# Kernel tuning notes

Hardware: AMD Instinct MI355X
Metric: run time of the kernel (lower is better)

## Reference

```python
import jax, jax.numpy as jnp
import numpy as np
import math

NUM_HEADS = 16
HEAD_DIM = 64
NUM_BUCKETS = 256
MAX_DISTANCE = 16384
ROPE_BASE = 10000.0


def _rel_pos_bucket(rel):
    # faithful to RelativePositionEncoding._relative_position_bucket
    ab = jnp.abs(rel)
    max_exact = NUM_BUCKETS // 4  # 64
    half = NUM_BUCKETS // 2       # 128
    is_small = ab < max_exact
    safe = jnp.maximum(ab, 1).astype(jnp.float32)
    large = max_exact + (jnp.log(safe / max_exact) / math.log(MAX_DISTANCE / max_exact) * (half - max_exact)).astype(jnp.int32)
    large = jnp.minimum(large, half - 1)
    bucket = jnp.where(is_small, ab, large)
    bucket = jnp.where(rel < 0, half + bucket, bucket)
    return bucket


def _rope_cos_sin(seq_len):
    # RotaryPositionEncoding with rope dim = 2*head_dim: num_features = head_dim,
    # inv_freq over arange(0, head_dim, 2)/head_dim, interleaved repeat to head_dim
    inv_freq = 1.0 / (ROPE_BASE ** (jnp.arange(0, HEAD_DIM, 2, dtype=jnp.float32) / HEAD_DIM))
    pos = jnp.arange(seq_len, dtype=jnp.float32)
    freqs = pos[:, None] * inv_freq[None, :]          # [S, HEAD_DIM//2]
    cos = jnp.repeat(jnp.cos(freqs), 2, axis=-1)      # [S, HEAD_DIM]
    sin = jnp.repeat(jnp.sin(freqs), 2, axis=-1)
    return cos, sin


def _rotate_half(t):
    h = t.shape[-1] // 2
    return jnp.concatenate([-t[..., h:], t[..., :h]], axis=-1)


def setup_inputs() -> dict:
    key = jax.random.key(0)
    ks = jax.random.split(key, 6)
    B, S, E = 2, 2048, 1024
    x = jax.random.normal(ks[0], (B, S, E), dtype=jnp.float32)
    Wq = jax.random.normal(ks[1], (E, E), dtype=jnp.float32) * 0.02
    Wk = jax.random.normal(ks[2], (E, E), dtype=jnp.float32) * 0.02
    Wv = jax.random.normal(ks[3], (E, E), dtype=jnp.float32) * 0.02
    Wo = jax.random.normal(ks[4], (E, E), dtype=jnp.float32) * 0.02
    rel_emb = jax.random.normal(ks[5], (NUM_BUCKETS, NUM_HEADS, HEAD_DIM), dtype=jnp.float32) * 0.02
    return {"x": x, "Wq": Wq, "Wk": Wk, "Wv": Wv, "Wo": Wo, "rel_emb": rel_emb}


def reference(x, Wq, Wk, Wv, Wo, rel_emb):
    B, S, E = x.shape
    H, D = NUM_HEADS, HEAD_DIM

    def split_heads(t):
        return t.reshape(B, S, H, D).transpose(0, 2, 1, 3)  # [B,H,S,D]

    q = split_heads(x @ Wq)
    k = split_heads(x @ Wk)
    v = split_heads(x @ Wv)

    # inline RoPE on q/k (cos/sin broadcast over batch & heads)
    cos, sin = _rope_cos_sin(S)  # [S, D]
    q = q * cos + _rotate_half(q) * sin
    k = k * cos + _rotate_half(k) * sin

    # relative-position bucket bias: q . rel_emb[bucket(i-j)]
    pos = jnp.arange(S)
    bucket = _rel_pos_bucket(pos[:, None] - pos[None, :])      # [S, S]
    q_rel = jnp.einsum('bhqd,nhd->bhqn', q, rel_emb)           # [B,H,S,NUM_BUCKETS]
    bias = jnp.take_along_axis(q_rel, bucket[None, None, :, :], axis=-1)  # [B,H,S,S]

    scale = 1.0 / math.sqrt(D)
    scores = (jnp.einsum('bhqd,bhkd->bhqk', q, k) + bias) * scale

    causal = pos[:, None] >= pos[None, :]
    scores = jnp.where(causal[None, None], scores, jnp.float32(-1e9))
    attn = jax.nn.softmax(scores, axis=-1)

    out = jnp.einsum('bhqk,bhkd->bhqd', attn, v)
    out = out.transpose(0, 2, 1, 3).reshape(B, S, E)
    return out @ Wo
```

## Files before the change

### kernel.cpp

```cpp
#include <hip/hip_runtime.h>
#include <hip/hip_bf16.h>
#include <math.h>


typedef __attribute__((ext_vector_type(8))) short bf16x8;
typedef __attribute__((ext_vector_type(4))) float f32x4;

static __device__ __forceinline__ unsigned short f2bf(float x) {
    unsigned u = __float_as_uint(x);
    unsigned r = (u + 0x7fffu + ((u >> 16) & 1u)) >> 16;
    return (unsigned short)r;
}
static __device__ __forceinline__ float bf2f(unsigned short h) {
    return __uint_as_float(((unsigned)h) << 16);
}

#define GLOAD16(gp, lp)                                                            \
    __builtin_amdgcn_global_load_lds(                                              \
        (const __attribute__((address_space(1))) unsigned int*)(gp),               \
        (__attribute__((address_space(3))) unsigned int*)(lp), 16, 0, 0)

__global__ void tobf16(const float* __restrict__ in, unsigned short* __restrict__ out)
{
    const size_t t = (size_t)blockIdx.x * 256 + threadIdx.x;
    const float4* p = (const float4*)(in + t*8);
    float4 a = p[0], b = p[1];
    unsigned w0 = f2bf(a.x) | ((unsigned)f2bf(a.y) << 16);
    unsigned w1 = f2bf(a.z) | ((unsigned)f2bf(a.w) << 16);
    unsigned w2 = f2bf(b.x) | ((unsigned)f2bf(b.y) << 16);
    unsigned w3 = f2bf(b.z) | ((unsigned)f2bf(b.w) << 16);
    *(uint4*)(out + t*8) = make_uint4(w0, w1, w2, w3);
}

__global__ void transp4(const float* __restrict__ W0, const float* __restrict__ W1,
                        const float* __restrict__ W2, const float* __restrict__ W3,
                        unsigned short* __restrict__ T0, unsigned short* __restrict__ T1,
                        unsigned short* __restrict__ T2, unsigned short* __restrict__ T3)
{
    const int z = blockIdx.y;
    const float* W = (z == 0) ? W0 : (z == 1) ? W1 : (z == 2) ? W2 : W3;
    unsigned short* Wt = (z == 0) ? T0 : (z == 1) ? T1 : (z == 2) ? T2 : T3;

    __shared__ unsigned short tls[64][65];
    const int tid = threadIdx.x;
    const int bxt = blockIdx.x & 15;
    const int byt = blockIdx.x >> 4;
    const int r   = tid >> 2;
    const int c0  = (tid & 3) * 16;
    const float* src = W + (size_t)(byt*64 + r)*1024 + bxt*64 + c0;
#pragma unroll
    for (int j = 0; j < 4; ++j) {
        float4 vv = ((const float4*)src)[j];
        tls[c0 + j*4 + 0][r] = f2bf(vv.x);
        tls[c0 + j*4 + 1][r] = f2bf(vv.y);
        tls[c0 + j*4 + 2][r] = f2bf(vv.z);
        tls[c0 + j*4 + 3][r] = f2bf(vv.w);
    }
    __syncthreads();
    unsigned short* dst = Wt + (size_t)(bxt*64 + r)*1024 + byt*64 + c0;
    unsigned w[8];
#pragma unroll
    for (int j = 0; j < 8; ++j)
        w[j] = (unsigned)tls[r][c0 + 2*j] | ((unsigned)tls[r][c0 + 2*j + 1] << 16);
    *(uint4*)(dst)     = make_uint4(w[0], w[1], w[2], w[3]);
    *(uint4*)(dst + 8) = make_uint4(w[4], w[5], w[6], w[7]);
}

__global__ void relT_bf(const float* __restrict__ rel, unsigned short* __restrict__ relTb)
{
    const int t  = blockIdx.x * 256 + threadIdx.x;
    const int d0 = (t & 7) * 8;
    const int n  = (t >> 3) & 127;
    const int h  = t >> 10;
    const float* src = rel + ((size_t)(n*16 + h))*64 + d0;
    float4 a = ((const float4*)src)[0], b = ((const float4*)src)[1];
    unsigned w0 = f2bf(a.x) | ((unsigned)f2bf(a.y) << 16);
    unsigned w1 = f2bf(a.z) | ((unsigned)f2bf(a.w) << 16);
    unsigned w2 = f2bf(b.x) | ((unsigned)f2bf(b.y) << 16);
    unsigned w3 = f2bf(b.z) | ((unsigned)f2bf(b.w) << 16);
    *(uint4*)(relTb + (size_t)h*8192 + n*64 + d0) = make_uint4(w0, w1, w2, w3);
}

#define GEMM_STAGE(t, buf)                                                             \
    {                                                                                  \
        const int k0s = (t) * 64;                                                      \
        _Pragma("unroll")                                                              \
        for (int j = 0; j < 4; ++j) {                                                  \
            GLOAD16(agp + (size_t)(j*32 + srow)*1024 + k0s, &Als[buf][0] + j*2048 + tid*8); \
            GLOAD16(bgp + (size_t)(j*32 + srow)*1024 + k0s, &Bls[buf][0] + j*2048 + tid*8); \
        }                                                                              \
    }

#define GEMM_COMPUTE(buf)                                                              \
    {                                                                                  \
        _Pragma("unroll")                                                              \
        for (int ks = 0; ks < 2; ++ks) {                                               \
            bf16x8 af[4], bfr[4];                                                      \
            _Pragma("unroll")                                                          \
            for (int m = 0; m < 4; ++m)                                                \
                af[m] = *(const bf16x8*)&Als[buf][(wr + m*16 + (lane & 15))*64 + ks*32 + (lane >> 4)*8]; \
            _Pragma("unroll")                                                          \
            for (int n = 0; n < 4; ++n)                                                \
                bfr[n] = *(const bf16x8*)&Bls[buf][(wc + n*16 + (lane & 15))*64 + ks*32 + (lane >> 4)*8]; \
            _Pragma("unroll")                                                          \
            for (int m = 0; m < 4; ++m)                                                \
                _Pragma("unroll")                                                      \
                for (int n = 0; n < 4; ++n)                                            \
                    acc[m][n] = __builtin_amdgcn_mfma_f32_16x16x32_bf16(af[m], bfr[n], acc[m][n], 0, 0, 0); \
        }                                                                              \
    }

__global__ __launch_bounds__(256) void gemm_qkv(const unsigned short* __restrict__ A,
    const unsigned short* __restrict__ wtq, const unsigned short* __restrict__ wtk,
    const unsigned short* __restrict__ wtv,
    float* __restrict__ qf, float* __restrict__ kf, unsigned short* __restrict__ vTb)
{
    __shared__ __align__(16) unsigned short Als[2][8192];
    __shared__ __align__(16) unsigned short Bls[2][8192];
    const int z = blockIdx.z;
    const unsigned short* Bt = (z == 0) ? wtq : (z == 1) ? wtk : wtv;

    const int tid  = threadIdx.x;
    const int wave = tid >> 6, lane = tid & 63;
    const int wr = (wave >> 1) * 64, wc = (wave & 1) * 64;
    const int bx = blockIdx.x, by = blockIdx.y;
    const int srow = tid >> 3;
    const unsigned short* agp = A  + (size_t)(by*128)*1024 + (tid & 7)*8;
    const unsigned short* bgp = Bt + (size_t)(bx*128)*1024 + (tid & 7)*8;

    f32x4 acc[4][4];
#pragma unroll
    for (int m = 0; m < 4; ++m)
#pragma unroll
        for (int n = 0; n < 4; ++n) acc[m][n] = (f32x4)0.f;

    GEMM_STAGE(0, 0);
    __syncthreads();
    int cur = 0;
    for (int t = 0; t < 16; ++t) {
        if (t < 15) GEMM_STAGE(t + 1, cur ^ 1);
        GEMM_COMPUTE(cur);
        __syncthreads();
        cur ^= 1;
    }

#pragma unroll
    for (int m = 0; m < 4; ++m) {
        const int r0 = by*128 + wr + m*16 + (lane >> 4)*4;
#pragma unroll
        for (int n = 0; n < 4; ++n) {
            const int col = bx*128 + wc + n*16 + (lane & 15);
            if (z == 2) {
                const int bb = r0 >> 11, ss = r0 & 2047;
                const int hh = col >> 6, dd = col & 63;
                unsigned r01 = f2bf(acc[m][n][0]) | ((unsigned)f2bf(acc[m][n][1]) << 16);
                unsigned r23 = f2bf(acc[m][n][2]) | ((unsigned)f2bf(acc[m][n][3]) << 16);
                *(uint2*)(vTb + (((size_t)bb*16 + hh)*64 + dd)*2048 + ss) = make_uint2(r01, r23);
            } else {
                float* C = z ? kf : qf;
#pragma unroll
                for (int rg = 0; rg < 4; ++rg) {
                    const int row = r0 + rg;
                    const int bb = row >> 11, ss = row & 2047;
                    const int hh = col >> 6,  dd = col & 63;
                    C[(((size_t)bb*16 + hh)*2048 + ss)*64 + dd] = acc[m][n][rg];
                }
            }
        }
    }
}

__global__ __launch_bounds__(256) void gemm_o(const unsigned short* __restrict__ A,
                                              const unsigned short* __restrict__ Bt,
                                              float* __restrict__ C)
{
    __shared__ __align__(16) unsigned short Als[2][8192];
    __shared__ __align__(16) unsigned short Bls[2][8192];
    const int tid  = threadIdx.x;
    const int wave = tid >> 6, lane = tid & 63;
    const int wr = (wave >> 1) * 64, wc = (wave & 1) * 64;
    const int bx = blockIdx.x, by = blockIdx.y;
    const int srow = tid >> 3;
    const unsigned short* agp = A  + (size_t)(by*128)*1024 + (tid & 7)*8;
    const unsigned short* bgp = Bt + (size_t)(bx*128)*1024 + (tid & 7)*8;

    f32x4 acc[4][4];
#pragma unroll
    for (int m = 0; m < 4; ++m)
#pragma unroll
        for (int n = 0; n < 4; ++n) acc[m][n] = (f32x4)0.f;

    GEMM_STAGE(0, 0);
    __syncthreads();
    int cur = 0;
    for (int t = 0; t < 16; ++t) {
        if (t < 15) GEMM_STAGE(t + 1, cur ^ 1);
        GEMM_COMPUTE(cur);
        __syncthreads();
        cur ^= 1;
    }

#pragma unroll
    for (int m = 0; m < 4; ++m) {
        const int r0 = by*128 + wr + m*16 + (lane >> 4)*4;
#pragma unroll
        for (int n = 0; n < 4; ++n) {
            const int col = bx*128 + wc + n*16 + (lane & 15);
#pragma unroll
            for (int rg = 0; rg < 4; ++rg)
                C[(size_t)(r0 + rg)*1024 + col] = acc[m][n][rg];
        }
    }
}

__global__ void rope_bf16(const float* __restrict__ qf, const float* __restrict__ kf,
                          unsigned short* __restrict__ qb, unsigned short* __restrict__ kb)
{
    const int t = blockIdx.x * 256 + threadIdx.x;
    const int ten = t >> 21;
    const int r = t & ((1 << 21) - 1);
    const int dd = r & 31;
    const int s  = (r >> 5) & 2047;
    const int bh = r >> 16;
    const float* p = ten ? kf : qf;
    unsigned short* o = ten ? kb : qb;
    const size_t base = ((size_t)bh*2048 + s)*64;
    const float x0 = p[base + dd];
    const float x1 = p[base + dd + 32];
    const float f0 = (float)(dd >> 1);
    const float CC = 0.41524101186092029f;
    const float if0 = exp2f(-f0 * CC);
    const float if1 = exp2f(-(f0 + 16.f) * CC);
    const float a0 = (float)s * if0;
    const float a1 = (float)s * if1;
    o[base + dd]      = f2bf(x0 * cosf(a0) - x1 * sinf(a0));
    o[base + dd + 32] = f2bf(x1 * cosf(a1) + x0 * sinf(a1));
}

__global__ __launch_bounds__(256) void qrel_mfma(const unsigned short* __restrict__ qb,
                                                 const unsigned short* __restrict__ relTb,
                                                 unsigned short* __restrict__ qrelb)
{
    __shared__ __align__(16) unsigned short Rls[8192];
    __shared__ __align__(16) unsigned short Qls[8192];
    const int tid  = threadIdx.x;
    const int wave = tid >> 6, lane = tid & 63;
    const int wr = (wave >> 1) * 64;
    const int wc = (wave & 1) * 64;
    const int s0 = blockIdx.x * 128;
    const int bh = blockIdx.y;
    const int h  = bh & 15;

    const unsigned short* qsrc = qb + ((size_t)bh*2048 + s0)*64;
    const unsigned short* rsrc = relTb + (size_t)h*8192;
#pragma unroll
    for (int j = 0; j < 4; ++j) {
        GLOAD16(rsrc + j*2048 + tid*8, &Rls[0] + j*2048 + tid*8);
        GLOAD16(qsrc + j*2048 + tid*8, &Qls[0] + j*2048 + tid*8);
    }

    f32x4 acc[4][4];
#pragma unroll
    for (int m = 0; m < 4; ++m)
#pragma unroll
        for (int n = 0; n < 4; ++n) acc[m][n] = (f32x4)0.f;

    __syncthreads();

#pragma unroll
    for (int ks = 0; ks < 2; ++ks) {
        bf16x8 rf[4], qf[4];
#pragma unroll
        for (int m = 0; m < 4; ++m)
            rf[m] = *(const bf16x8*)&Rls[(wr + m*16 + (lane & 15))*64 + ks*32 + (lane >> 4)*8];
#pragma unroll
        for (int n = 0; n < 4; ++n)
            qf[n] = *(const bf16x8*)&Qls[(wc + n*16 + (lane & 15))*64 + ks*32 + (lane >> 4)*8];
#pragma unroll
        for (int m = 0; m < 4; ++m)
#pragma unroll
            for (int n = 0; n < 4; ++n)
                acc[m][n] = __builtin_amdgcn_mfma_f32_16x16x32_bf16(rf[m], qf[n], acc[m][n], 0, 0, 0);
    }

#pragma unroll
    for (int m = 0; m < 4; ++m) {
        const int bkt0 = wr + m*16 + (lane >> 4)*4;
#pragma unroll
        for (int n = 0; n < 4; ++n) {
            const int srow = s0 + wc + n*16 + (lane & 15);
            unsigned r01 = f2bf(acc[m][n][0]) | ((unsigned)f2bf(acc[m][n][1]) << 16);
            unsigned r23 = f2bf(acc[m][n][2]) | ((unsigned)f2bf(acc[m][n][3]) << 16);
            *(uint2*)(qrelb + ((size_t)bh*2048 + srow)*128 + bkt0) = make_uint2(r01, r23);
        }
    }
}

__global__ __launch_bounds__(256) void flash_mfma(
    const unsigned short* __restrict__ qb, const unsigned short* __restrict__ kb,
    const unsigned short* __restrict__ vT, const unsigned short* __restrict__ qrelb,
    unsigned short* __restrict__ ctxb)
{
    __shared__ __align__(16) unsigned short kls[4096];
    __shared__ __align__(16) unsigned short vtls[4096];
    __shared__ __align__(16) unsigned short qrels[64*136];
    __shared__ unsigned char btbl[2048];

    const int tid = threadIdx.x;
    const int id  = blockIdx.x;
    const int bh  = id & 31;
    const int mm  = id >> 5;
    const int aa  = mm & 7, bgrp = mm >> 3;
    const int bx  = 8*bgrp + ((bgrp & 1) ? 7 - aa : aa);
    const int i0  = bx * 64;

    const int w   = tid >> 6;
    const int l   = tid & 63;
    const int q15 = l & 15;
    const int g   = l >> 4;
    const int iq  = i0 + w*16 + q15;

    for (int idx = tid; idx < 2048; idx += 256) {
        int bkt;
        if (idx < 64) bkt = idx;
        else {
            bkt = 64 + (int)(__log2f((float)idx) * 8.0f - 48.0f);
            bkt = bkt > 127 ? 127 : bkt;
        }
        btbl[idx] = (unsigned char)bkt;
    }
    for (int idx = tid; idx < 1024; idx += 256) {
        const int r = idx >> 4, c8 = idx & 15;
        uint4 vv = *(const uint4*)(qrelb + ((size_t)bh*2048 + i0 + r)*128 + c8*8);
        *(uint4*)&qrels[r*136 + c8*8] = vv;
    }

    bf16x8 qf0, qf1;
    {
        const unsigned short* qrow = qb + ((size_t)bh*2048 + i0 + w*16 + q15)*64;
        qf0 = *(const bf16x8*)(qrow + g*8);
        qf1 = *(const bf16x8*)(qrow + 32 + g*8);
    }

    f32x4 acc[4];
#pragma unroll
    for (int d = 0; d < 4; ++d) acc[d] = (f32x4)0.f;
    float mrun = -INFINITY, lsum = 0.f;

    const size_t headoff = (size_t)bh * 2048 * 64;
    const unsigned short* gbase;
    int jstride;
    char* lbase;
    if (tid < 128) { gbase = kb + headoff; jstride = 64; lbase = (char*)kls; }
    else           { gbase = vT + headoff; jstride = 1;  lbase = (char*)vtls; }
    int soff[4]; char* ldst[4];
#pragma unroll
    for (int i = 0; i < 4; ++i) {
        const int D = (tid & 127)*16 + i*2048;
        const int r = D >> 7, c = (D >> 4) & 7;
        soff[i] = (tid < 128) ? (r*64 + ((c ^ (r & 7))*8))
                              : (r*2048 + ((c ^ (r & 7))*8));
        ldst[i] = lbase + D;
    }

    const int ntiles = bx + 1;
    const float SCL = 0.1803368801111204f;
    const int qrow_lds = (w*16 + q15) * 136;
    const int srcA = ((2*g) & 3)*16 + q15;
    const int srcB = ((2*g + 1) & 3)*16 + q15;

    for (int t = 0; t < ntiles; ++t) {
        const int j0 = t * 64;
        __syncthreads();
        {
            const unsigned short* gt = gbase + (size_t)j0 * jstride;
#pragma unroll
            for (int i = 0; i < 4; ++i) GLOAD16(gt + soff[i], ldst[i]);
        }
        __syncthreads();

        f32x4 s[4];
#pragma unroll
        for (int ss = 0; ss < 4; ++ss) s[ss] = (f32x4)0.f;
#pragma unroll
        for (int ks = 0; ks < 2; ++ks) {
            const bf16x8 qq = ks ? qf1 : qf0;
            const int gr = ((ks*4 + g) ^ (q15 & 7)) * 8;
#pragma unroll
            for (int ss = 0; ss < 4; ++ss) {
                bf16x8 kf = *(const bf16x8*)&kls[(ss*16 + q15)*64 + gr];
                s[ss] = __builtin_amdgcn_mfma_f32_16x16x32_bf16(kf, qq, s[ss], 0, 0, 0);
            }
        }
        float sv[16];
        float tmax = -INFINITY;
#pragma unroll
        for (int ss = 0; ss < 4; ++ss) {
#pragma unroll
            for (int r = 0; r < 4; ++r) {
                const int rel = iq - (j0 + ss*16 + g*4 + r);
                const int bi = rel < 0 ? 0 : rel;
                const float bias = bf2f(qrels[qrow_lds + btbl[bi]]);
                const float val = (s[ss][r] + bias) * SCL;
                sv[ss*4 + r] = (rel >= 0) ? val : -1e30f;
                tmax = fmaxf(tmax, sv[ss*4 + r]);
            }
        }
        tmax = fmaxf(tmax, __shfl_xor(tmax, 16));
        tmax = fmaxf(tmax, __shfl_xor(tmax, 32));

        float newm = mrun;
        if (!__all(tmax - mrun <= 8.0f)) {
            newm = fmaxf(mrun, tmax);
            const float corr = exp2f(mrun - newm);
            lsum *= corr;
#pragma unroll
            for (int d = 0; d < 4; ++d) {
                acc[d][0] *= corr; acc[d][1] *= corr; acc[d][2] *= corr; acc[d][3] *= corr;
            }
            mrun = newm;
        }

        float p[16], ps = 0.f;
#pragma unroll
        for (int j = 0; j < 16; ++j) { p[j] = exp2f(sv[j] - newm); ps += p[j]; }
        ps += __shfl_xor(ps, 16);
        ps += __shfl_xor(ps, 32);
        lsum += ps;

#pragma unroll
        for (int ck = 0; ck < 2; ++ck) {
            unsigned w00 = f2bf(p[8*ck+0]) | ((unsigned)f2bf(p[8*ck+1]) << 16);
            unsigned w01 = f2bf(p[8*ck+2]) | ((unsigned)f2bf(p[8*ck+3]) << 16);
            unsigned w10 = f2bf(p[8*ck+4]) | ((unsigned)f2bf(p[8*ck+5]) << 16);
            unsigned w11 = f2bf(p[8*ck+6]) | ((unsigned)f2bf(p[8*ck+7]) << 16);
            unsigned a0 = (unsigned)__shfl((int)w00, srcA);
            unsigned b0 = (unsigned)__shfl((int)w10, srcA);
            unsigned a1 = (unsigned)__shfl((int)w01, srcA);
            unsigned b1 = (unsigned)__shfl((int)w11, srcA);
            unsigned a2 = (unsigned)__shfl((int)w00, srcB);
            unsigned b2 = (unsigned)__shfl((int)w10, srcB);
            unsigned a3 = (unsigned)__shfl((int)w01, srcB);
            unsigned b3 = (unsigned)__shfl((int)w11, srcB);
            union { unsigned u[4]; bf16x8 v; } pu;
            pu.u[0] = (g < 2) ? a0 : b0;
            pu.u[1] = (g < 2) ? a1 : b1;
            pu.u[2] = (g < 2) ? a2 : b2;
            pu.u[3] = (g < 2) ? a3 : b3;
#pragma unroll
            for (int dblk = 0; dblk < 4; ++dblk) {
                const int d2 = dblk*16 + q15;
                bf16x8 vf = *(const bf16x8*)&vtls[d2*64 + (((ck*4 + g) ^ (d2 & 7))*8)];
                acc[dblk] = __builtin_amdgcn_mfma_f32_16x16x32_bf16(vf, pu.v, acc[dblk], 0, 0, 0);
            }
        }
    }

    const float inv = 1.0f / lsum;
    const int s2 = i0 + w*16 + q15;
    const int b2 = bh >> 4, hh = bh & 15;
    unsigned short* obase = ctxb + (((size_t)b2*2048 + s2)*16 + hh)*64;
#pragma unroll
    for (int dblk = 0; dblk < 4; ++dblk) {
        const int d0 = dblk*16 + g*4;
        unsigned r01 = f2bf(acc[dblk][0]*inv) | ((unsigned)f2bf(acc[dblk][1]*inv) << 16);
        unsigned r23 = f2bf(acc[dblk][2]*inv) | ((unsigned)f2bf(acc[dblk][3]*inv) << 16);
        *(uint2*)(obase + d0) = make_uint2(r01, r23);
    }
}

extern "C" void kernel_launch(void* const* d_in, const int* in_sizes, int n_in,
                              void* d_out, int out_size, void* d_ws, size_t ws_size,
                              hipStream_t stream)
{
    const float* x   = (const float*)d_in[0];
    const float* Wq  = (const float*)d_in[1];
    const float* Wk  = (const float*)d_in[2];
    const float* Wv  = (const float*)d_in[3];
    const float* Wo  = (const float*)d_in[4];
    const float* rel = (const float*)d_in[5];

    float* ws = (float*)d_ws;
    float* qf32 = ws;
    float* kf32 = ws + 4194304;
    unsigned short* qb    = (unsigned short*)(ws + 8388608);
    unsigned short* kbb   = (unsigned short*)(ws + 10485760);
    unsigned short* qrelb = (unsigned short*)(ws + 12582912);
    unsigned short* vTb   = (unsigned short*)(ws + 16777216);
    unsigned short* xb    = (unsigned short*)(ws + 18874368);
    unsigned short* wtq   = (unsigned short*)(ws + 20971520);
    unsigned short* wtk   = (unsigned short*)(ws + 21495808);
    unsigned short* wtv   = (unsigned short*)(ws + 22020096);
    unsigned short* wto   = (unsigned short*)(ws + 22544384);
    unsigned short* relTb = (unsigned short*)(ws + 23068672);
    unsigned short* ctxb  = (unsigned short*)ws;

    tobf16<<<2048, 256, 0, stream>>>(x, xb);
    transp4<<<dim3(256, 4), 256, 0, stream>>>(Wq, Wk, Wv, Wo, wtq, wtk, wtv, wto);
    relT_bf<<<64, 256, 0, stream>>>(rel, relTb);

    gemm_qkv<<<dim3(8, 32, 3), 256, 0, stream>>>(xb, wtq, wtk, wtv, qf32, kf32, vTb);
    rope_bf16<<<16384, 256, 0, stream>>>(qf32, kf32, qb, kbb);
    qrel_mfma<<<dim3(16, 32), 256, 0, stream>>>(qb, relTb, qrelb);
    flash_mfma<<<1024, 256, 0, stream>>>(qb, kbb, vTb, qrelb, ctxb);
    gemm_o<<<dim3(8, 32), 256, 0, stream>>>(ctxb, wto, (float*)d_out);
}
```

Measured before the change: 208.9 us.

## Fuse prep kernels, pair causal query tiles per block, use hardware bf16 convert

Merges the three preprocessing kernels (x cast, weight transposes, rel-embedding cast) into one launch. The flash kernel now runs 512 blocks, each handling two complementary query tiles (px and 31-px) so every block does the same number of causal key tiles. The bucket lookup table in LDS is replaced by inline log2 computation. Software bf16 rounding is replaced by the v_cvt_pk_bf16_f32 instruction, and exp2f by the raw exp2 intrinsic. Halving the block count may reduce occupancy and latency hiding, and the inline bucket math adds ALU work to the inner loop.

```diff
diff --git a/kernel.cpp b/kernel.cpp
--- a/kernel.cpp
+++ b/kernel.cpp
@@ -14,71 +14,77 @@
 static __device__ __forceinline__ float bf2f(unsigned short h) {
     return __uint_as_float(((unsigned)h) << 16);
 }
+static __device__ __forceinline__ unsigned cvtpk(float lo, float hi) {
+    unsigned r;
+    asm("v_cvt_pk_bf16_f32 %0, %1, %2" : "=v"(r) : "v"(lo), "v"(hi));
+    return r;
+}
+static __device__ __forceinline__ float fexp2(float x) {
+    return __builtin_amdgcn_exp2f(x);
+}
 
 #define GLOAD16(gp, lp)                                                            \
     __builtin_amdgcn_global_load_lds(                                              \
         (const __attribute__((address_space(1))) unsigned int*)(gp),               \
         (__attribute__((address_space(3))) unsigned int*)(lp), 16, 0, 0)
 
-__global__ void tobf16(const float* __restrict__ in, unsigned short* __restrict__ out)
-{
-    const size_t t = (size_t)blockIdx.x * 256 + threadIdx.x;
-    const float4* p = (const float4*)(in + t*8);
-    float4 a = p[0], b = p[1];
-    unsigned w0 = f2bf(a.x) | ((unsigned)f2bf(a.y) << 16);
-    unsigned w1 = f2bf(a.z) | ((unsigned)f2bf(a.w) << 16);
-    unsigned w2 = f2bf(b.x) | ((unsigned)f2bf(b.y) << 16);
-    unsigned w3 = f2bf(b.z) | ((unsigned)f2bf(b.w) << 16);
-    *(uint4*)(out + t*8) = make_uint4(w0, w1, w2, w3);
-}
-
-__global__ void transp4(const float* __restrict__ W0, const float* __restrict__ W1,
-                        const float* __restrict__ W2, const float* __restrict__ W3,
-                        unsigned short* __restrict__ T0, unsigned short* __restrict__ T1,
-                        unsigned short* __restrict__ T2, unsigned short* __restrict__ T3)
-{
-    const int z = blockIdx.y;
-    const float* W = (z == 0) ? W0 : (z == 1) ? W1 : (z == 2) ? W2 : W3;
-    unsigned short* Wt = (z == 0) ? T0 : (z == 1) ? T1 : (z == 2) ? T2 : T3;
-
+__global__ void prep(const float* __restrict__ x,
+                     const float* __restrict__ W0, const float* __restrict__ W1,
+                     const float* __restrict__ W2, const float* __restrict__ W3,
+                     const float* __restrict__ rel,
+                     unsigned short* __restrict__ xb,
+                     unsigned short* __restrict__ T0, unsigned short* __restrict__ T1,
+                     unsigned short* __restrict__ T2, unsigned short* __restrict__ T3,
+                     unsigned short* __restrict__ relTb)
+{
     __shared__ unsigned short tls[64][65];
+    const int id  = blockIdx.x;
     const int tid = threadIdx.x;
-    const int bxt = blockIdx.x & 15;
-    const int byt = blockIdx.x >> 4;
-    const int r   = tid >> 2;
-    const int c0  = (tid & 3) * 16;
-    const float* src = W + (size_t)(byt*64 + r)*1024 + bxt*64 + c0;
-#pragma unroll
-    for (int j = 0; j < 4; ++j) {
-        float4 vv = ((const float4*)src)[j];
-        tls[c0 + j*4 + 0][r] = f2bf(vv.x);
-        tls[c0 + j*4 + 1][r] = f2bf(vv.y);
-        tls[c0 + j*4 + 2][r] = f2bf(vv.z);
-        tls[c0 + j*4 + 3][r] = f2bf(vv.w);
-    }
-    __syncthreads();
-    unsigned short* dst = Wt + (size_t)(bxt*64 + r)*1024 + byt*64 + c0;
-    unsigned w[8];
-#pragma unroll
-    for (int j = 0; j < 8; ++j)
-        w[j] = (unsigned)tls[r][c0 + 2*j] | ((unsigned)tls[r][c0 + 2*j + 1] << 16);
-    *(uint4*)(dst)     = make_uint4(w[0], w[1], w[2], w[3]);
-    *(uint4*)(dst + 8) = make_uint4(w[4], w[5], w[6], w[7]);
-}
-
-__global__ void relT_bf(const float* __restrict__ rel, unsigned short* __restrict__ relTb)
-{
-    const int t  = blockIdx.x * 256 + threadIdx.x;
-    const int d0 = (t & 7) * 8;
-    const int n  = (t >> 3) & 127;
-    const int h  = t >> 10;
-    const float* src = rel + ((size_t)(n*16 + h))*64 + d0;
-    float4 a = ((const float4*)src)[0], b = ((const float4*)src)[1];
-    unsigned w0 = f2bf(a.x) | ((unsigned)f2bf(a.y) << 16);
-    unsigned w1 = f2bf(a.z) | ((unsigned)f2bf(a.w) << 16);
-    unsigned w2 = f2bf(b.x) | ((unsigned)f2bf(b.y) << 16);
-    unsigned w3 = f2bf(b.z) | ((unsigned)f2bf(b.w) << 16);
-    *(uint4*)(relTb + (size_t)h*8192 + n*64 + d0) = make_uint4(w0, w1, w2, w3);
+    if (id < 2048) {
+        const size_t t = (size_t)id * 256 + tid;
+        const float4* p = (const float4*)(x + t*8);
+        float4 a = p[0], b = p[1];
+        unsigned w0 = cvtpk(a.x, a.y), w1 = cvtpk(a.z, a.w);
+        unsigned w2 = cvtpk(b.x, b.y), w3 = cvtpk(b.z, b.w);
+        *(uint4*)(xb + t*8) = make_uint4(w0, w1, w2, w3);
+    } else if (id < 3072) {
+        const int local = id - 2048;
+        const int z  = local >> 8;
+        const float* W = (z == 0) ? W0 : (z == 1) ? W1 : (z == 2) ? W2 : W3;
+        unsigned short* Wt = (z == 0) ? T0 : (z == 1) ? T1 : (z == 2) ? T2 : T3;
+        const int bb  = local & 255;
+        const int bxt = bb & 15;
+        const int byt = bb >> 4;
+        const int r   = tid >> 2;
+        const int c0  = (tid & 3) * 16;
+        const float* src = W + (size_t)(byt*64 + r)*1024 + bxt*64 + c0;
+#pragma unroll
+        for (int j = 0; j < 4; ++j) {
+            float4 vv = ((const float4*)src)[j];
+            tls[c0 + j*4 + 0][r] = f2bf(vv.x);
+            tls[c0 + j*4 + 1][r] = f2bf(vv.y);
+            tls[c0 + j*4 + 2][r] = f2bf(vv.z);
+            tls[c0 + j*4 + 3][r] = f2bf(vv.w);
+        }
+        __syncthreads();
+        unsigned short* dst = Wt + (size_t)(bxt*64 + r)*1024 + byt*64 + c0;
+        unsigned w[8];
+#pragma unroll
+        for (int j = 0; j < 8; ++j)
+            w[j] = (unsigned)tls[r][c0 + 2*j] | ((unsigned)tls[r][c0 + 2*j + 1] << 16);
+        *(uint4*)(dst)     = make_uint4(w[0], w[1], w[2], w[3]);
+        *(uint4*)(dst + 8) = make_uint4(w[4], w[5], w[6], w[7]);
+    } else {
+        const int t  = (id - 3072) * 256 + tid;
+        const int d0 = (t & 7) * 8;
+        const int n  = (t >> 3) & 127;
+        const int h  = t >> 10;
+        const float* src = rel + ((size_t)(n*16 + h))*64 + d0;
+        float4 a = ((const float4*)src)[0], b = ((const float4*)src)[1];
+        unsigned w0 = cvtpk(a.x, a.y), w1 = cvtpk(a.z, a.w);
+        unsigned w2 = cvtpk(b.x, b.y), w3 = cvtpk(b.z, b.w);
+        *(uint4*)(relTb + (size_t)h*8192 + n*64 + d0) = make_uint4(w0, w1, w2, w3);
+    }
 }
 
 #define GEMM_STAGE(t, buf)                                                             \
@@ -153,8 +159,8 @@
             if (z == 2) {
                 const int bb = r0 >> 11, ss = r0 & 2047;
                 const int hh = col >> 6, dd = col & 63;
-                unsigned r01 = f2bf(acc[m][n][0]) | ((unsigned)f2bf(acc[m][n][1]) << 16);
-                unsigned r23 = f2bf(acc[m][n][2]) | ((unsigned)f2bf(acc[m][n][3]) << 16);
+                unsigned r01 = cvtpk(acc[m][n][0], acc[m][n][1]);
+                unsigned r23 = cvtpk(acc[m][n][2], acc[m][n][3]);
                 *(uint2*)(vTb + (((size_t)bb*16 + hh)*64 + dd)*2048 + ss) = make_uint2(r01, r23);
             } else {
                 float* C = z ? kf : qf;
@@ -289,8 +295,8 @@
 #pragma unroll
         for (int n = 0; n < 4; ++n) {
             const int srow = s0 + wc + n*16 + (lane & 15);
-            unsigned r01 = f2bf(acc[m][n][0]) | ((unsigned)f2bf(acc[m][n][1]) << 16);
-            unsigned r23 = f2bf(acc[m][n][2]) | ((unsigned)f2bf(acc[m][n][3]) << 16);
+            unsigned r01 = cvtpk(acc[m][n][0], acc[m][n][1]);
+            unsigned r23 = cvtpk(acc[m][n][2], acc[m][n][3]);
             *(uint2*)(qrelb + ((size_t)bh*2048 + srow)*128 + bkt0) = make_uint2(r01, r23);
         }
     }
@@ -304,48 +310,16 @@
     __shared__ __align__(16) unsigned short kls[4096];
     __shared__ __align__(16) unsigned short vtls[4096];
     __shared__ __align__(16) unsigned short qrels[64*136];
-    __shared__ unsigned char btbl[2048];
 
     const int tid = threadIdx.x;
     const int id  = blockIdx.x;
     const int bh  = id & 31;
-    const int mm  = id >> 5;
-    const int aa  = mm & 7, bgrp = mm >> 3;
-    const int bx  = 8*bgrp + ((bgrp & 1) ? 7 - aa : aa);
-    const int i0  = bx * 64;
+    const int px  = id >> 5;
 
     const int w   = tid >> 6;
     const int l   = tid & 63;
     const int q15 = l & 15;
     const int g   = l >> 4;
-    const int iq  = i0 + w*16 + q15;
-
-    for (int idx = tid; idx < 2048; idx += 256) {
-        int bkt;
-        if (idx < 64) bkt = idx;
-        else {
-            bkt = 64 + (int)(__log2f((float)idx) * 8.0f - 48.0f);
-            bkt = bkt > 127 ? 127 : bkt;
-        }
-        btbl[idx] = (unsigned char)bkt;
-    }
-    for (int idx = tid; idx < 1024; idx += 256) {
-        const int r = idx >> 4, c8 = idx & 15;
-        uint4 vv = *(const uint4*)(qrelb + ((size_t)bh*2048 + i0 + r)*128 + c8*8);
-        *(uint4*)&qrels[r*136 + c8*8] = vv;
-    }
-
-    bf16x8 qf0, qf1;
-    {
-        const unsigned short* qrow = qb + ((size_t)bh*2048 + i0 + w*16 + q15)*64;
-        qf0 = *(const bf16x8*)(qrow + g*8);
-        qf1 = *(const bf16x8*)(qrow + 32 + g*8);
-    }
-
-    f32x4 acc[4];
-#pragma unroll
-    for (int d = 0; d < 4; ++d) acc[d] = (f32x4)0.f;
-    float mrun = -INFINITY, lsum = 0.f;
 
     const size_t headoff = (size_t)bh * 2048 * 64;
     const unsigned short* gbase;
@@ -363,109 +337,140 @@
         ldst[i] = lbase + D;
     }
 
-    const int ntiles = bx + 1;
     const float SCL = 0.1803368801111204f;
     const int qrow_lds = (w*16 + q15) * 136;
     const int srcA = ((2*g) & 3)*16 + q15;
     const int srcB = ((2*g + 1) & 3)*16 + q15;
 
-    for (int t = 0; t < ntiles; ++t) {
-        const int j0 = t * 64;
+    for (int pp = 0; pp < 2; ++pp) {
+        const int bxc = pp ? (31 - px) : px;
+        const int i0  = bxc * 64;
+        const int iq  = i0 + w*16 + q15;
+
         __syncthreads();
+        for (int idx = tid; idx < 1024; idx += 256) {
+            const int r = idx >> 4, c8 = idx & 15;
+            uint4 vv = *(const uint4*)(qrelb + ((size_t)bh*2048 + i0 + r)*128 + c8*8);
+            *(uint4*)&qrels[r*136 + c8*8] = vv;
+        }
+
+        bf16x8 qf0, qf1;
         {
-            const unsigned short* gt = gbase + (size_t)j0 * jstride;
-#pragma unroll
-            for (int i = 0; i < 4; ++i) GLOAD16(gt + soff[i], ldst[i]);
-        }
-        __syncthreads();
-
-        f32x4 s[4];
-#pragma unroll
-        for (int ss = 0; ss < 4; ++ss) s[ss] = (f32x4)0.f;
-#pragma unroll
-        for (int ks = 0; ks < 2; ++ks) {
-            const bf16x8 qq = ks ? qf1 : qf0;
-            const int gr = ((ks*4 + g) ^ (q15 & 7)) * 8;
+            const unsigned short* qrow = qb + ((size_t)bh*2048 + i0 + w*16 + q15)*64;
+            qf0 = *(const bf16x8*)(qrow + g*8);
+            qf1 = *(const bf16x8*)(qrow + 32 + g*8);
+        }
+
+        f32x4 acc[4];
+#pragma unroll
+        for (int d = 0; d < 4; ++d) acc[d] = (f32x4)0.f;
+        float mrun = -INFINITY, lsum = 0.f;
+
+        const int ntiles = bxc + 1;
+        for (int t = 0; t < ntiles; ++t) {
+            const int j0 = t * 64;
+            __syncthreads();
+            {
+                const unsigned short* gt = gbase + (size_t)j0 * jstride;
+#pragma unroll
+                for (int i = 0; i < 4; ++i) GLOAD16(gt + soff[i], ldst[i]);
+            }
+            __syncthreads();
+
+            f32x4 s[4];
+#pragma unroll
+            for (int ss = 0; ss < 4; ++ss) s[ss] = (f32x4)0.f;
+#pragma unroll
+            for (int ks = 0; ks < 2; ++ks) {
+                const bf16x8 qq = ks ? qf1 : qf0;
+                const int gr = ((ks*4 + g) ^ (q15 & 7)) * 8;
+#pragma unroll
+                for (int ss = 0; ss < 4; ++ss) {
+                    bf16x8 kf = *(const bf16x8*)&kls[(ss*16 + q15)*64 + gr];
+                    s[ss] = __builtin_amdgcn_mfma_f32_16x16x32_bf16(kf, qq, s[ss], 0, 0, 0);
+                }
+            }
+            float sv[16];
+            float tmax = -INFINITY;
 #pragma unroll
             for (int ss = 0; ss < 4; ++ss) {
-                bf16x8 kf = *(const bf16x8*)&kls[(ss*16 + q15)*64 + gr];
-                s[ss] = __builtin_amdgcn_mfma_f32_16x16x32_bf16(kf, qq, s[ss], 0, 0, 0);
+#pragma unroll
+                for (int r = 0; r < 4; ++r) {
+                    const int rel = iq - (j0 + ss*16 + g*4 + r);
+                    const int bi = rel < 0 ? 0 : rel;
+                    int bkt;
+                    if (bi < 64) bkt = bi;
+                    else {
+                        bkt = 64 + (int)(__log2f((float)bi) * 8.0f - 48.0f);
+                        bkt = bkt > 127 ? 127 : bkt;
+                    }
+                    const float bias = bf2f(qrels[qrow_lds + bkt]);
+                    const float val = (s[ss][r] + bias) * SCL;
+                    sv[ss*4 + r] = (rel >= 0) ? val : -1e30f;
+                    tmax = fmaxf(tmax, sv[ss*4 + r]);
+                }
             }
-        }
-        float sv[16];
-        float tmax = -INFINITY;
-#pragma unroll
-        for (int ss = 0; ss < 4; ++ss) {
-#pragma unroll
-            for (int r = 0; r < 4; ++r) {
-                const int rel = iq - (j0 + ss*16 + g*4 + r);
-                const int bi = rel < 0 ? 0 : rel;
-                const float bias = bf2f(qrels[qrow_lds + btbl[bi]]);
-                const float val = (s[ss][r] + bias) * SCL;
-                sv[ss*4 + r] = (rel >= 0) ? val : -1e30f;
-                tmax = fmaxf(tmax, sv[ss*4 + r]);
+            tmax = fmaxf(tmax, __shfl_xor(tmax, 16));
+            tmax = fmaxf(tmax, __shfl_xor(tmax, 32));
+
+            float newm = mrun;
+            if (!__all(tmax - mrun <= 8.0f)) {
+                newm = fmaxf(mrun, tmax);
+                const float corr = fexp2(mrun - newm);
+                lsum *= corr;
+#pragma unroll
+                for (int d = 0; d < 4; ++d) {
+                    acc[d][0] *= corr; acc[d][1] *= corr; acc[d][2] *= corr; acc[d][3] *= corr;
+                }
+                mrun = newm;
             }
-        }
-        tmax = fmaxf(tmax, __shfl_xor(tmax, 16));
-        tmax = fmaxf(tmax, __shfl_xor(tmax, 32));
-
-        float newm = mrun;
-        if (!__all(tmax - mrun <= 8.0f)) {
-            newm = fmaxf(mrun, tmax);
-            const float corr = exp2f(mrun - newm);
-            lsum *= corr;
-#pragma unroll
-            for (int d = 0; d < 4; ++d) {
-                acc[d][0] *= corr; acc[d][1] *= corr; acc[d][2] *= corr; acc[d][3] *= corr;
+
+            float p[16], ps = 0.f;
+#pragma unroll
+            for (int j = 0; j < 16; ++j) { p[j] = fexp2(sv[j] - newm); ps += p[j]; }
+            ps += __shfl_xor(ps, 16);
+            ps += __shfl_xor(ps, 32);
+            lsum += ps;
+
+#pragma unroll
+            for (int ck = 0; ck < 2; ++ck) {
+                unsigned w00 = cvtpk(p[8*ck+0], p[8*ck+1]);
+                unsigned w01 = cvtpk(p[8*ck+2], p[8*ck+3]);
+                unsigned w10 = cvtpk(p[8*ck+4], p[8*ck+5]);
+                unsigned w11 = cvtpk(p[8*ck+6], p[8*ck+7]);
+                unsigned a0 = (unsigned)__shfl((int)w00, srcA);
+                unsigned b0 = (unsigned)__shfl((int)w10, srcA);
+                unsigned a1 = (unsigned)__shfl((int)w01, srcA);
+                unsigned b1 = (unsigned)__shfl((int)w11, srcA);
+                unsigned a2 = (unsigned)__shfl((int)w00, srcB);
+                unsigned b2 = (unsigned)__shfl((int)w10, srcB);
+                unsigned a3 = (unsigned)__shfl((int)w01, srcB);
+                unsigned b3 = (unsigned)__shfl((int)w11, srcB);
+                union { unsigned u[4]; bf16x8 v; } pu;
+                pu.u[0] = (g < 2) ? a0 : b0;
+                pu.u[1] = (g < 2) ? a1 : b1;
+                pu.u[2] = (g < 2) ? a2 : b2;
+                pu.u[3] = (g < 2) ? a3 : b3;
+#pragma unroll
+                for (int dblk = 0; dblk < 4; ++dblk) {
+                    const int d2 = dblk*16 + q15;
+                    bf16x8 vf = *(const bf16x8*)&vtls[d2*64 + (((ck*4 + g) ^ (d2 & 7))*8)];
+                    acc[dblk] = __builtin_amdgcn_mfma_f32_16x16x32_bf16(vf, pu.v, acc[dblk], 0, 0, 0);
+                }
             }
-            mrun = newm;
-        }
-
-        float p[16], ps = 0.f;
-#pragma unroll
-        for (int j = 0; j < 16; ++j) { p[j] = exp2f(sv[j] - newm); ps += p[j]; }
-        ps += __shfl_xor(ps, 16);
-        ps += __shfl_xor(ps, 32);
-        lsum += ps;
-
-#pragma unroll
-        for (int ck = 0; ck < 2; ++ck) {
-            unsigned w00 = f2bf(p[8*ck+0]) | ((unsigned)f2bf(p[8*ck+1]) << 16);
-            unsigned w01 = f2bf(p[8*ck+2]) | ((unsigned)f2bf(p[8*ck+3]) << 16);
-            unsigned w10 = f2bf(p[8*ck+4]) | ((unsigned)f2bf(p[8*ck+5]) << 16);
-            unsigned w11 = f2bf(p[8*ck+6]) | ((unsigned)f2bf(p[8*ck+7]) << 16);
-            unsigned a0 = (unsigned)__shfl((int)w00, srcA);
-            unsigned b0 = (unsigned)__shfl((int)w10, srcA);
-            unsigned a1 = (unsigned)__shfl((int)w01, srcA);
-            unsigned b1 = (unsigned)__shfl((int)w11, srcA);
-            unsigned a2 = (unsigned)__shfl((int)w00, srcB);
-            unsigned b2 = (unsigned)__shfl((int)w10, srcB);
-            unsigned a3 = (unsigned)__shfl((int)w01, srcB);
-            unsigned b3 = (unsigned)__shfl((int)w11, srcB);
-            union { unsigned u[4]; bf16x8 v; } pu;
-            pu.u[0] = (g < 2) ? a0 : b0;
-            pu.u[1] = (g < 2) ? a1 : b1;
-            pu.u[2] = (g < 2) ? a2 : b2;
-            pu.u[3] = (g < 2) ? a3 : b3;
-#pragma unroll
-            for (int dblk = 0; dblk < 4; ++dblk) {
-                const int d2 = dblk*16 + q15;
-                bf16x8 vf = *(const bf16x8*)&vtls[d2*64 + (((ck*4 + g) ^ (d2 & 7))*8)];
-                acc[dblk] = __builtin_amdgcn_mfma_f32_16x16x32_bf16(vf, pu.v, acc[dblk], 0, 0, 0);
-            }
-        }
-    }
-
-    const float inv = 1.0f / lsum;
-    const int s2 = i0 + w*16 + q15;
-    const int b2 = bh >> 4, hh = bh & 15;
-    unsigned short* obase = ctxb + (((size_t)b2*2048 + s2)*16 + hh)*64;
-#pragma unroll
-    for (int dblk = 0; dblk < 4; ++dblk) {
-        const int d0 = dblk*16 + g*4;
-        unsigned r01 = f2bf(acc[dblk][0]*inv) | ((unsigned)f2bf(acc[dblk][1]*inv) << 16);
-        unsigned r23 = f2bf(acc[dblk][2]*inv) | ((unsigned)f2bf(acc[dblk][3]*inv) << 16);
-        *(uint2*)(obase + d0) = make_uint2(r01, r23);
+        }
+
+        const float inv = 1.0f / lsum;
+        const int s2 = i0 + w*16 + q15;
+        const int b2 = bh >> 4, hh = bh & 15;
+        unsigned short* obase = ctxb + (((size_t)b2*2048 + s2)*16 + hh)*64;
+#pragma unroll
+        for (int dblk = 0; dblk < 4; ++dblk) {
+            const int d0 = dblk*16 + g*4;
+            unsigned r01 = cvtpk(acc[dblk][0]*inv, acc[dblk][1]*inv);
+            unsigned r23 = cvtpk(acc[dblk][2]*inv, acc[dblk][3]*inv);
+            *(uint2*)(obase + d0) = make_uint2(r01, r23);
+        }
     }
 }
 
@@ -495,13 +500,10 @@
     unsigned short* relTb = (unsigned short*)(ws + 23068672);
     unsigned short* ctxb  = (unsigned short*)ws;
 
-    tobf16<<<2048, 256, 0, stream>>>(x, xb);
-    transp4<<<dim3(256, 4), 256, 0, stream>>>(Wq, Wk, Wv, Wo, wtq, wtk, wtv, wto);
-    relT_bf<<<64, 256, 0, stream>>>(rel, relTb);
-
+    prep<<<3136, 256, 0, stream>>>(x, Wq, Wk, Wv, Wo, rel, xb, wtq, wtk, wtv, wto, relTb);
     gemm_qkv<<<dim3(8, 32, 3), 256, 0, stream>>>(xb, wtq, wtk, wtv, qf32, kf32, vTb);
     rope_bf16<<<16384, 256, 0, stream>>>(qf32, kf32, qb, kbb);
     qrel_mfma<<<dim3(16, 32), 256, 0, stream>>>(qb, relTb, qrelb);
-    flash_mfma<<<1024, 256, 0, stream>>>(qb, kbb, vTb, qrelb, ctxb);
+    flash_mfma<<<512, 256, 0, stream>>>(qb, kbb, vTb, qrelb, ctxb);
     gemm_o<<<dim3(8, 32), 256, 0, stream>>>(ctxb, wto, (float*)d_out);
 }
```

New measurement: 205.0 us. No clear change (-1.9%).
